# Kernel tuning notes

Hardware: AMD Instinct MI355X
Metric: run time of the kernel (lower is better)

## Reference

```python
import jax, jax.numpy as jnp
import numpy as np

N_NODES = 100000
N_GRAPHS = 1000
NPG = 100           # nodes per graph (fixed)
N_EDGES = 3200000   # avg degree 32
F_IN = 128
K = 30              # SortAggregation k
N_CLASSES = 10


def setup_inputs() -> dict:
    key = jax.random.key(0)
    ks = jax.random.split(key, 24)
    x = jax.random.normal(ks[0], (N_NODES, F_IN), jnp.float32)
    # edges constrained within each 100-node graph
    g = jax.random.randint(ks[1], (N_EDGES,), 0, N_GRAPHS)
    src = g * NPG + jax.random.randint(ks[2], (N_EDGES,), 0, NPG)
    dst = g * NPG + jax.random.randint(ks[3], (N_EDGES,), 0, NPG)
    edge_index = jnp.stack([src, dst]).astype(jnp.int32)
    batch = jnp.repeat(jnp.arange(N_GRAPHS, dtype=jnp.int32), NPG)

    def lin(k, fi, fo):
        return jax.random.normal(k, (fi, fo), jnp.float32) / np.sqrt(fi)

    return {
        "x": x, "edge_index": edge_index, "batch": batch,
        "W1": lin(ks[4], F_IN, 32), "b1": jnp.zeros((32,), jnp.float32),
        "W2": lin(ks[5], 32, 32),   "b2": jnp.zeros((32,), jnp.float32),
        "W3": lin(ks[6], 32, 32),   "b3": jnp.zeros((32,), jnp.float32),
        "W4": lin(ks[7], 32, 1),    "b4": jnp.zeros((1,), jnp.float32),
        "conv5_w": jax.random.normal(ks[8], (16, 1, 97), jnp.float32) / np.sqrt(97.0),
        "conv5_b": jnp.zeros((16,), jnp.float32),
        "conv6_w": jax.random.normal(ks[9], (32, 16, 5), jnp.float32) / np.sqrt(16 * 5.0),
        "conv6_b": jnp.zeros((32,), jnp.float32),
        "fc1_w": lin(ks[10], 352, 128), "fc1_b": jnp.zeros((128,), jnp.float32),
        "fc2_w": lin(ks[11], 128, N_CLASSES), "fc2_b": jnp.zeros((N_CLASSES,), jnp.float32),
    }


def reference(x, edge_index, batch,
              W1, b1, W2, b2, W3, b3, W4, b4,
              conv5_w, conv5_b, conv6_w, conv6_b,
              fc1_w, fc1_b, fc2_w, fc2_b):
    N = x.shape[0]
    src, dst = edge_index[0], edge_index[1]
    # remove_self_loops -> zero edge weight; GCNConv then re-adds self loops (weight 1)
    w = jnp.where(src == dst, 0.0, 1.0).astype(x.dtype)
    deg = jax.ops.segment_sum(w, dst, num_segments=N) + 1.0  # includes self loop
    dis = jax.lax.rsqrt(deg)
    norm = w * dis[src] * dis[dst]        # per-edge D^-1/2 A D^-1/2
    self_norm = dis * dis                 # self-loop coefficient 1/deg

    def gcn(h, W, b):
        h = h @ W                                   # [N, out]
        agg = jax.ops.segment_sum(norm[:, None] * h[src], dst, num_segments=N)
        return agg + self_norm[:, None] * h + b

    x1 = jnp.tanh(gcn(x, W1, b1))
    x2 = jnp.tanh(gcn(x1, W2, b2))
    x3 = jnp.tanh(gcn(x2, W3, b3))
    x4 = jnp.tanh(gcn(x3, W4, b4))
    h = jnp.concatenate([x1, x2, x3, x4], axis=-1)  # [N, 97]
    C = h.shape[-1]

    # SortAggregation(k=30): per graph, sort nodes by last channel descending, keep top k
    xs = h.reshape(N_GRAPHS, NPG, C)
    order = jnp.argsort(-xs[..., -1], axis=1)[:, :K]            # [B, K]
    pooled = jnp.take_along_axis(xs, order[:, :, None], axis=1)  # [B, K, C]
    y = pooled.reshape(N_GRAPHS, 1, K * C)                       # [B, 1, 2910]

    dn = ('NCH', 'OIH', 'NCH')
    y = jax.lax.conv_general_dilated(y, conv5_w, (97,), 'VALID', dimension_numbers=dn)
    y = jax.nn.relu(y + conv5_b[None, :, None])                  # [B, 16, 30]
    B, Co, L = y.shape
    y = y.reshape(B, Co, L // 2, 2).max(axis=-1)                 # maxpool(2,2) -> [B,16,15]
    y = jax.lax.conv_general_dilated(y, conv6_w, (1,), 'VALID', dimension_numbers=dn)
    y = jax.nn.relu(y + conv6_b[None, :, None])                  # [B, 32, 11]
    y = y.reshape(B, -1)                                         # [B, 352]
    out = jax.nn.relu(y @ fc1_w + fc1_b)                         # dropout = identity (eval)
    return jax.nn.log_softmax(out @ fc2_w + fc2_b, axis=-1)
```

## Files before the change

### kernel.cpp

```cpp
#include <hip/hip_runtime.h>

#define N_GRAPHS_C 1000
#define NPG_C      100
#define N_EDGES_C  3200000
#define KTOP_C     30
#define CAP        4096

typedef _Float16 f16x8 __attribute__((ext_vector_type(8)));
typedef float    f32x4 __attribute__((ext_vector_type(4)));

__device__ __forceinline__ unsigned packh2(float x, float y) {
    _Float16 hx = (_Float16)x, hy = (_Float16)y;
    return (unsigned)__builtin_bit_cast(unsigned short, hx) |
           ((unsigned)__builtin_bit_cast(unsigned short, hy) << 16);
}

__device__ __forceinline__ float f16b(unsigned v) {
    return (float)__builtin_bit_cast(_Float16, (unsigned short)v);
}

__device__ __forceinline__ float ftanh(float x) {
    float e = __expf(2.0f * x);
    return 1.0f - 2.0f * __builtin_amdgcn_rcpf(e + 1.0f);
}

__device__ __forceinline__ void split8(const float* v, f16x8& h, f16x8& l) {
    #pragma unroll
    for (int j = 0; j < 8; ++j) {
        _Float16 hh = (_Float16)v[j];
        h[j] = hh;
        l[j] = (_Float16)(v[j] - (float)hh);
    }
}


__global__ __launch_bounds__(1024)
void bucket_kernel(const int* __restrict__ src, const int* __restrict__ dst,
                   int* __restrict__ gcur, unsigned short* __restrict__ slots) {
    __shared__ int hist[N_GRAPHS_C];
    const int tid = threadIdx.x;
    const int base = blockIdx.x * 8192;
    for (int i = tid; i < N_GRAPHS_C; i += 1024) hist[i] = 0;
    __syncthreads();

    int g[8]; unsigned short pk[8]; bool v[8];
    #pragma unroll
    for (int k = 0; k < 8; ++k) {
        int e = base + tid + k * 1024;
        v[k] = false;
        if (e < N_EDGES_C) {
            int s = src[e], d = dst[e];
            if (s != d) {
                int gg = s / NPG_C;
                g[k] = gg;
                pk[k] = (unsigned short)(((d - gg * NPG_C) << 7) | (s - gg * NPG_C));
                v[k] = true;
                atomicAdd(&hist[gg], 1);
            }
        }
    }
    __syncthreads();
    for (int i = tid; i < N_GRAPHS_C; i += 1024) {
        int c = hist[i];
        hist[i] = atomicAdd(&gcur[i], c);
    }
    __syncthreads();
    #pragma unroll
    for (int k = 0; k < 8; ++k) {
        if (v[k]) {
            int pos = atomicAdd(&hist[g[k]], 1);
            if (pos < CAP) slots[g[k] * CAP + pos] = pk[k];
        }
    }
}

__global__ __launch_bounds__(512)
void wprep_kernel(const float* __restrict__ W1, const float* __restrict__ W2,
                  const float* __restrict__ W3, unsigned* __restrict__ wp) {
    const int t = threadIdx.x;
    for (int w = t; w < 2048; w += 512) {
        int n = w >> 6, kp = w & 63, k = kp * 2;
        float a = W1[k*32 + n], b = W1[(k+1)*32 + n];
        _Float16 ah = (_Float16)a, bh = (_Float16)b;
        wp[w]        = (unsigned)__builtin_bit_cast(unsigned short, ah) |
                       ((unsigned)__builtin_bit_cast(unsigned short, bh) << 16);
        wp[2048 + w] = packh2(a - (float)ah, b - (float)bh);
    }
    for (int w = t; w < 512; w += 512) {
        int n = w >> 4, kp = w & 15, k = kp * 2;
        float a = W2[k*32 + n], b = W2[(k+1)*32 + n];
        _Float16 ah = (_Float16)a, bh = (_Float16)b;
        wp[4096 + w] = (unsigned)__builtin_bit_cast(unsigned short, ah) |
                       ((unsigned)__builtin_bit_cast(unsigned short, bh) << 16);
        wp[4608 + w] = packh2(a - (float)ah, b - (float)bh);
    }
    for (int w = t; w < 512; w += 512) {
        int n = w >> 4, kp = w & 15, k = kp * 2;
        float a = W3[k*32 + n], b = W3[(k+1)*32 + n];
        _Float16 ah = (_Float16)a, bh = (_Float16)b;
        wp[5120 + w] = (unsigned)__builtin_bit_cast(unsigned short, ah) |
                       ((unsigned)__builtin_bit_cast(unsigned short, bh) << 16);
        wp[5632 + w] = packh2(a - (float)ah, b - (float)bh);
    }
}

#define SMEM_WORDS 16112

extern "C" __global__ __launch_bounds__(512, 4)
void dgcnn_kernel(const float* __restrict__ x,
                  const int* __restrict__ gcur, const unsigned short* __restrict__ slots,
                  const unsigned* __restrict__ wp,
                  const float* __restrict__ b1, const float* __restrict__ b2,
                  const float* __restrict__ b3,
                  const float* __restrict__ W4, const float* __restrict__ b4,
                  const float* __restrict__ w5, const float* __restrict__ b5,
                  const float* __restrict__ w6, const float* __restrict__ b6,
                  const float* __restrict__ fw1, const float* __restrict__ fb1,
                  const float* __restrict__ fw2, const float* __restrict__ fb2,
                  float* __restrict__ out)
{
    extern __shared__ unsigned smu[];
    unsigned* cntP   = smu;
    unsigned* planes = smu + 7616;
    float* xrows  = (float*)(smu + 11968);
    float* pooled = (float*)(smu + 11968);
    float* dis = (float*)(smu + 15568);
    float* t4  = (float*)(smu + 15680);
    unsigned* t4h = smu + 15784;
    unsigned* t4l = smu + 15848;
    float* sX4 = (float*)(smu + 15912);
    int*   srank = (int*)(smu + 16012);
    float* s5  = (float*)smu;
    float* sPb = s5 + 480;
    float* s6  = s5 + 720;
    float* sO1 = s5 + 1072;
    float* sFc = s5 + 1200;
    float* sZ  = s5 + 1712;
    float* w5s = (float*)(smu + 1728);
    float* b5s = (float*)(smu + 3280);
    float* w6s = (float*)(smu + 3296);
    float* b6s = (float*)(smu + 5856);
    float* fw2s = (float*)(smu + 7616);
    float* fb2s = (float*)(smu + 8896);

    const int tid = threadIdx.x;
    const int g   = blockIdx.x;
    const int l64 = tid & 63;
    const int wv  = tid >> 6;

    const float* xg = x + (size_t)g * NPG_C * 128;
    const unsigned* w1h = wp;
    const unsigned* w1l = wp + 2048;

    for (int idx = tid; idx < 11968; idx += 512) smu[idx] = 0u;
    if (tid < 12) dis[100 + tid] = 0.f;
    if (tid < 100) srank[tid] = 0;
    __syncthreads();

    {
        int ec = gcur[g]; if (ec > CAP) ec = CAP;
        for (int k = tid; k < ec; k += 512) {
            unsigned e = slots[g * CAP + k];
            unsigned idx = (e >> 7) * 104 + (e & 127);
            atomicAdd(&planes[idx >> 2], 1u << ((idx & 3) * 8));
        }
    }
    __syncthreads();

    if (tid < 400) {
        int row = tid >> 2, part = tid & 3;
        int wb = part * 7, we = (part == 3) ? 26 : wb + 7;
        const unsigned* rw = planes + row * 26;
        unsigned s = 0;
        for (int k = wb; k < we; ++k) {
            unsigned v = rw[k];
            s += (v & 0xffu) + ((v >> 8) & 0xffu) + ((v >> 16) & 0xffu) + (v >> 24);
        }
        atomicAdd(&srank[row], (int)s);
    }
    __syncthreads();

    #pragma unroll
    for (int k = 0; k < 6; ++k) {
        int w = tid + k * 512;
        if (w < 2600) {
            unsigned v = planes[w];
            int i = w / 26, c = w - i * 26;
            int d = i * 68 + c * 2;
            cntP[d]     = packh2((float)(v & 255u), (float)((v >> 8) & 255u));
            cntP[d + 1] = packh2((float)((v >> 16) & 255u), (float)(v >> 24));
        }
    }
    if (tid < 100) dis[tid] = rsqrtf((float)srank[tid] + 1.0f);
    __syncthreads();

    auto packStore = [&](f32x4 c, int n, int r0, float4 dv) {
        float v0 = c[0]*dv.x, v1 = c[1]*dv.y, v2 = c[2]*dv.z, v3 = c[3]*dv.w;
        _Float16 h0=(_Float16)v0, h1=(_Float16)v1, h2=(_Float16)v2, h3=(_Float16)v3;
        uint2 wh, wl;
        wh.x = (unsigned)__builtin_bit_cast(unsigned short,h0) |
               ((unsigned)__builtin_bit_cast(unsigned short,h1) << 16);
        wh.y = (unsigned)__builtin_bit_cast(unsigned short,h2) |
               ((unsigned)__builtin_bit_cast(unsigned short,h3) << 16);
        wl.x = packh2(v0-(float)h0, v1-(float)h1);
        wl.y = packh2(v2-(float)h2, v3-(float)h3);
        *(uint2*)&planes[n*68 + (r0>>1)] = wh;
        *(uint2*)&planes[2176 + n*68 + (r0>>1)] = wl;
    };

    for (int idx = tid; idx < 768; idx += 512) {
        int rw = idx / 12, wd = idx - rw * 12;
        planes[rw * 68 + 56 + wd] = 0u;
    }
    if (wv < 7) {
        f32x4 c0 = {0.f,0.f,0.f,0.f}, c1 = {0.f,0.f,0.f,0.f};
        const int arow = (wv << 4) + (l64 & 15);
        const int kq   = (l64 >> 4) << 3;
        const int bn   = l64 & 15;
        const bool aok = arow < 100;
        #pragma unroll
        for (int kc = 0; kc < 4; ++kc) {
            const int kb = (kc << 5) + kq;
            f16x8 ah, al;
            if (aok) {
                float av[8];
                float4 xa = *(const float4*)&xg[arow*128 + kb];
                float4 xb = *(const float4*)&xg[arow*128 + kb + 4];
                av[0]=xa.x; av[1]=xa.y; av[2]=xa.z; av[3]=xa.w;
                av[4]=xb.x; av[5]=xb.y; av[6]=xb.z; av[7]=xb.w;
                split8(av, ah, al);
            } else {
                #pragma unroll
                for (int j = 0; j < 8; ++j) { ah[j] = (_Float16)0.f; al[j] = (_Float16)0.f; }
            }
            f16x8 b0h = __builtin_bit_cast(f16x8, *(const uint4*)(w1h + bn*64 + (kb>>1)));
            f16x8 b0l = __builtin_bit_cast(f16x8, *(const uint4*)(w1l + bn*64 + (kb>>1)));
            f16x8 b1h = __builtin_bit_cast(f16x8, *(const uint4*)(w1h + (bn+16)*64 + (kb>>1)));
            f16x8 b1l = __builtin_bit_cast(f16x8, *(const uint4*)(w1l + (bn+16)*64 + (kb>>1)));
            c0 = __builtin_amdgcn_mfma_f32_16x16x32_f16(ah, b0h, c0, 0, 0, 0);
            c0 = __builtin_amdgcn_mfma_f32_16x16x32_f16(al, b0h, c0, 0, 0, 0);
            c0 = __builtin_amdgcn_mfma_f32_16x16x32_f16(ah, b0l, c0, 0, 0, 0);
            c1 = __builtin_amdgcn_mfma_f32_16x16x32_f16(ah, b1h, c1, 0, 0, 0);
            c1 = __builtin_amdgcn_mfma_f32_16x16x32_f16(al, b1h, c1, 0, 0, 0);
            c1 = __builtin_amdgcn_mfma_f32_16x16x32_f16(ah, b1l, c1, 0, 0, 0);
        }
        const int r0 = (wv << 4) + ((l64 >> 4) << 2);
        float4 dv = *(const float4*)&dis[r0];
        packStore(c0, bn,      r0, dv);
        packStore(c1, bn + 16, r0, dv);
    }
    __syncthreads();

    auto AGG = [&](f32x4& fa, f32x4& fb, const float* Bp, bool wx) {
        if (wv < 7) {
            f32x4 a0 = {0.f,0.f,0.f,0.f}, a1 = {0.f,0.f,0.f,0.f};
            const unsigned* ab = cntP + ((wv << 4) + (l64 & 15)) * 68 + ((l64 >> 4) << 2);
            const unsigned* bb = planes + (l64 & 15) * 68 + ((l64 >> 4) << 2);
            #pragma unroll
            for (int p = 0; p < 2; ++p) {
                const unsigned* bp = bb + p * 2176;
                #pragma unroll
                for (int ks = 0; ks < 4; ++ks) {
                    f16x8 av = __builtin_bit_cast(f16x8, *(const uint4*)(ab + ks*16));
                    f16x8 b0 = __builtin_bit_cast(f16x8, *(const uint4*)(bp + ks*16));
                    f16x8 b1 = __builtin_bit_cast(f16x8, *(const uint4*)(bp + 16*68 + ks*16));
                    a0 = __builtin_amdgcn_mfma_f32_16x16x32_f16(av, b0, a0, 0, 0, 0);
                    a1 = __builtin_amdgcn_mfma_f32_16x16x32_f16(av, b1, a1, 0, 0, 0);
                }
            }
            int n0 = l64 & 15, r0 = (wv << 4) + ((l64 >> 4) << 2);
            uint2 sh0 = *(const uint2*)(planes + n0 * 68 + (r0 >> 1));
            uint2 sl0 = *(const uint2*)(planes + 2176 + n0 * 68 + (r0 >> 1));
            uint2 sh1 = *(const uint2*)(planes + (16 + n0) * 68 + (r0 >> 1));
            uint2 sl1 = *(const uint2*)(planes + 2176 + (16 + n0) * 68 + (r0 >> 1));
            float4 dv = *(const float4*)&dis[r0];
            float bi0 = Bp[n0], bi1 = Bp[16 + n0];
            #pragma unroll
            for (int j = 0; j < 4; ++j) {
                unsigned sft = (unsigned)((j & 1) * 16);
                float sc0 = f16b(((j < 2) ? sh0.x : sh0.y) >> sft) +
                            f16b(((j < 2) ? sl0.x : sl0.y) >> sft);
                float sc1 = f16b(((j < 2) ? sh1.x : sh1.y) >> sft) +
                            f16b(((j < 2) ? sl1.x : sl1.y) >> sft);
                float d_ = (j == 0) ? dv.x : (j == 1) ? dv.y : (j == 2) ? dv.z : dv.w;
                float v0 = ftanh(d_ * (a0[j] + sc0) + bi0);
                float v1 = ftanh(d_ * (a1[j] + sc1) + bi1);
                fa[j] = v0; fb[j] = v1;
                if (wx) {
                    int row = r0 + j;
                    if (row < 100) { xrows[row*36 + n0] = v0; xrows[row*36 + 16 + n0] = v1; }
                }
            }
        }
    };

    auto XWm = [&](const unsigned* wh, const unsigned* wl) {
        if (wv < 7) {
            f32x4 c0 = {0.f,0.f,0.f,0.f}, c1 = {0.f,0.f,0.f,0.f};
            const int arow = (wv << 4) + (l64 & 15);
            const int kq   = (l64 >> 4) << 3;
            const int bn   = l64 & 15;
            f16x8 ah, al;
            if (arow < 100) {
                float av[8];
                float4 xa = *(const float4*)&xrows[arow*36 + kq];
                float4 xb = *(const float4*)&xrows[arow*36 + kq + 4];
                av[0]=xa.x; av[1]=xa.y; av[2]=xa.z; av[3]=xa.w;
                av[4]=xb.x; av[5]=xb.y; av[6]=xb.z; av[7]=xb.w;
                split8(av, ah, al);
            } else {
                #pragma unroll
                for (int j = 0; j < 8; ++j) { ah[j] = (_Float16)0.f; al[j] = (_Float16)0.f; }
            }
            f16x8 b0h = __builtin_bit_cast(f16x8, *(const uint4*)(wh + bn*16 + (kq>>1)));
            f16x8 b0l = __builtin_bit_cast(f16x8, *(const uint4*)(wl + bn*16 + (kq>>1)));
            f16x8 b1h = __builtin_bit_cast(f16x8, *(const uint4*)(wh + (bn+16)*16 + (kq>>1)));
            f16x8 b1l = __builtin_bit_cast(f16x8, *(const uint4*)(wl + (bn+16)*16 + (kq>>1)));
            c0 = __builtin_amdgcn_mfma_f32_16x16x32_f16(ah, b0h, c0, 0, 0, 0);
            c0 = __builtin_amdgcn_mfma_f32_16x16x32_f16(al, b0h, c0, 0, 0, 0);
            c0 = __builtin_amdgcn_mfma_f32_16x16x32_f16(ah, b0l, c0, 0, 0, 0);
            c1 = __builtin_amdgcn_mfma_f32_16x16x32_f16(ah, b1h, c1, 0, 0, 0);
            c1 = __builtin_amdgcn_mfma_f32_16x16x32_f16(al, b1h, c1, 0, 0, 0);
            c1 = __builtin_amdgcn_mfma_f32_16x16x32_f16(ah, b1l, c1, 0, 0, 0);
            const int r0 = (wv << 4) + ((l64 >> 4) << 2);
            float4 dv = *(const float4*)&dis[r0];
            packStore(c0, bn,      r0, dv);
            packStore(c1, bn + 16, r0, dv);
        }
    };

    f32x4 f1a, f1b, f2a, f2b, f3a, f3b;

    AGG(f1a, f1b, b1, true);        __syncthreads();
    XWm(wp + 4096, wp + 4608);      __syncthreads();
    AGG(f2a, f2b, b2, true);        __syncthreads();
    XWm(wp + 5120, wp + 5632);      __syncthreads();
    AGG(f3a, f3b, b3, false);

    if (wv < 7) {
        float w4a = W4[l64 & 15], w4b = W4[16 + (l64 & 15)];
        int r0 = (wv << 4) + ((l64 >> 4) << 2);
        #pragma unroll
        for (int j = 0; j < 4; ++j) {
            float v = f3a[j] * w4a + f3b[j] * w4b;
            v += __shfl_xor(v, 1, 16); v += __shfl_xor(v, 2, 16);
            v += __shfl_xor(v, 4, 16); v += __shfl_xor(v, 8, 16);
            int row = r0 + j;
            if ((l64 & 15) == 0 && row < 100) t4[row] = v * dis[row];
        }
    }
    __syncthreads();

    if (tid < 64) {
        float a = (2*tid < 100) ? t4[2*tid] : 0.f;
        float b = (2*tid+1 < 100) ? t4[2*tid+1] : 0.f;
        _Float16 ah = (_Float16)a, bh = (_Float16)b;
        t4h[tid] = (unsigned)__builtin_bit_cast(unsigned short, ah) |
                   ((unsigned)__builtin_bit_cast(unsigned short, bh) << 16);
        t4l[tid] = packh2(a - (float)ah, b - (float)bh);
    }
    if (tid < 100) srank[tid] = 0;
    __syncthreads();

    if (wv < 7) {
        f32x4 c = {0.f,0.f,0.f,0.f};
        const unsigned* ab = cntP + ((wv << 4) + (l64 & 15)) * 68 + ((l64 >> 4) << 2);
        const int kq = (l64 >> 4) << 3;
        const bool bz = (l64 & 15) == 0;
        #pragma unroll
        for (int ks = 0; ks < 4; ++ks) {
            f16x8 av = __builtin_bit_cast(f16x8, *(const uint4*)(ab + ks*16));
            f16x8 bh, bl;
            if (bz) {
                bh = __builtin_bit_cast(f16x8, *(const uint4*)(t4h + ks*16 + (kq>>1)));
                bl = __builtin_bit_cast(f16x8, *(const uint4*)(t4l + ks*16 + (kq>>1)));
            } else {
                #pragma unroll
                for (int j = 0; j < 8; ++j) { bh[j] = (_Float16)0.f; bl[j] = (_Float16)0.f; }
            }
            c = __builtin_amdgcn_mfma_f32_16x16x32_f16(av, bh, c, 0, 0, 0);
            c = __builtin_amdgcn_mfma_f32_16x16x32_f16(av, bl, c, 0, 0, 0);
        }
        if (bz) {
            int r0 = (wv << 4) + ((l64 >> 4) << 2);
            #pragma unroll
            for (int j = 0; j < 4; ++j) {
                int row = r0 + j;
                if (row < 100) sX4[row] = tanhf(dis[row] * (c[j] + t4[row]) + b4[0]);
            }
        }
    }
    __syncthreads();

    if (tid < 500) {
        int i = tid / 5, seg = tid - i * 5;
        float vi = sX4[i];
        int c = 0, jb = seg * 20;
        #pragma unroll
        for (int jo = 0; jo < 20; ++jo) {
            int j = jb + jo;
            float vj = sX4[j];
            c += (vj > vi) || (vj == vi && j < i);
        }
        atomicAdd(&srank[i], c);
    }
    for (int k = tid; k < 1552; k += 512) w5s[k] = w5[k];
    if (tid < 16)  b5s[tid] = b5[tid];
    for (int k = tid; k < 2560; k += 512) w6s[k] = w6[k];
    if (tid < 32)  b6s[tid] = b6[tid];
    for (int k = tid; k < 1280; k += 512) fw2s[k] = fw2[k];
    if (tid < 10)  fb2s[tid] = fb2[tid];
    __syncthreads();

    if (wv < 7) {
        int n0 = l64 & 15, r0 = (wv << 4) + ((l64 >> 4) << 2);
        #pragma unroll
        for (int j = 0; j < 4; ++j) {
            int row = r0 + j;
            if (row < 100) {
                int rk = srank[row];
                if (rk < KTOP_C) {
                    float* pr = pooled + rk * 100;
                    pr[n0]      = f1a[j]; pr[16 + n0] = f1b[j];
                    pr[32 + n0] = f2a[j]; pr[48 + n0] = f2b[j];
                    pr[64 + n0] = f3a[j]; pr[80 + n0] = f3b[j];
                    if (n0 == 0) pr[96] = sX4[row];
                }
            }
        }
    }
    __syncthreads();

    if (tid < 480) {
        int l = tid >> 4, co = tid & 15;
        const float* pr = pooled + l * 100;
        const float* wr = w5s + co * 97;
        float acc = b5s[co];
        for (int c4 = 0; c4 < 96; c4 += 4) {
            const float4 pv = *(const float4*)&pr[c4];
            acc = fmaf(pv.x, wr[c4+0], fmaf(pv.y, wr[c4+1], fmaf(pv.z, wr[c4+2], fmaf(pv.w, wr[c4+3], acc))));
        }
        acc = fmaf(pr[96], wr[96], acc);
        s5[co * 30 + l] = fmaxf(acc, 0.f);
    }
    __syncthreads();

    if (tid < 240) {
        int co = tid / 15, j = tid - co * 15;
        sPb[co * 15 + j] = fmaxf(s5[co * 30 + 2*j], s5[co * 30 + 2*j + 1]);
    }
    __syncthreads();

    if (tid < 352) {
        int co = tid / 11, l = tid - co * 11;
        float acc = b6s[co];
        for (int ci = 0; ci < 16; ++ci) {
            const float* wr = w6s + (co * 16 + ci) * 5;
            const float* pr = sPb + ci * 15 + l;
            acc = fmaf(wr[0], pr[0], fmaf(wr[1], pr[1], fmaf(wr[2], pr[2],
                  fmaf(wr[3], pr[3], fmaf(wr[4], pr[4], acc)))));
        }
        s6[co * 11 + l] = fmaxf(acc, 0.f);
    }
    __syncthreads();

    {
        int j = tid & 127, part = tid >> 7;
        int ibeg = part * 88, iend = ibeg + 88;
        float acc = (part == 0) ? fb1[j] : 0.f;
        for (int i = ibeg; i < iend; ++i)
            acc = fmaf(s6[i], fw1[i * 128 + j], acc);
        sFc[part * 128 + j] = acc;
    }
    __syncthreads();
    if (tid < 128) {
        float v = sFc[tid] + sFc[128 + tid] + sFc[256 + tid] + sFc[384 + tid];
        sO1[tid] = fmaxf(v, 0.f);
    }
    __syncthreads();

    if (tid < 10) {
        float acc = fb2s[tid];
        for (int k = 0; k < 128; ++k)
            acc = fmaf(sO1[k], fw2s[k * 10 + tid], acc);
        sZ[tid] = acc;
    }
    __syncthreads();
    if (tid < 10) {
        float m = sZ[0];
        for (int c = 1; c < 10; ++c) m = fmaxf(m, sZ[c]);
        float se = 0.f;
        for (int c = 0; c < 10; ++c) se += expf(sZ[c] - m);
        out[g * 10 + tid] = sZ[tid] - m - logf(se);
    }
}

extern "C" void kernel_launch(void* const* d_in, const int* in_sizes, int n_in,
                              void* d_out, int out_size, void* d_ws, size_t ws_size,
                              hipStream_t stream) {
    const float* x   = (const float*)d_in[0];
    const int*   ei  = (const int*)d_in[1];
    const int*   src = ei;
    const int*   dst = ei + N_EDGES_C;
    const float* W1 = (const float*)d_in[3];  const float* b1 = (const float*)d_in[4];
    const float* W2 = (const float*)d_in[5];  const float* b2 = (const float*)d_in[6];
    const float* W3 = (const float*)d_in[7];  const float* b3 = (const float*)d_in[8];
    const float* W4 = (const float*)d_in[9];  const float* b4 = (const float*)d_in[10];
    const float* w5 = (const float*)d_in[11]; const float* b5 = (const float*)d_in[12];
    const float* w6 = (const float*)d_in[13]; const float* b6 = (const float*)d_in[14];
    const float* fw1 = (const float*)d_in[15]; const float* fb1 = (const float*)d_in[16];
    const float* fw2 = (const float*)d_in[17]; const float* fb2 = (const float*)d_in[18];
    float* out = (float*)d_out;

    int* gcur = (int*)d_ws;
    unsigned short* slots = (unsigned short*)((char*)d_ws + 4096);
    unsigned* wpp = (unsigned*)((char*)d_ws + 4096 + (size_t)N_GRAPHS_C * CAP * 2);

    hipMemsetAsync(gcur, 0, 4096, stream);

    bucket_kernel<<<(N_EDGES_C + 8191) / 8192, 1024, 0, stream>>>(src, dst, gcur, slots);
    wprep_kernel<<<1, 512, 0, stream>>>(W1, W2, W3, wpp);

    size_t smem = (size_t)SMEM_WORDS * sizeof(unsigned);
    hipFuncSetAttribute((const void*)dgcnn_kernel,
                        hipFuncAttributeMaxDynamicSharedMemorySize, (int)smem);
    dgcnn_kernel<<<N_GRAPHS_C, 512, smem, stream>>>(
        x, gcur, slots, wpp, b1, b2, b3, W4, b4,
        w5, b5, w6, b6, fw1, fb1, fw2, fb2, out);
}
```

Baseline: 110.1 us.

## Keep adjacency A-fragments in registers and shrink LDS to double occupancy

Removes the fp16 count-matrix copy (cntP) in LDS and instead builds the MFMA A-operand fragments for the adjacency once into registers, reused by all aggregation steps. Conv/FC weights are read directly from global memory instead of being staged into shared memory, cutting the LDS footprint roughly in half and raising launch bounds to 8 blocks per CU. The weight-prep kernel is merged into the bucket kernel as an extra block to save a launch. Risks are higher register pressure from the held fragments and uncached global weight reads in the tail layers.

Result: faster. 106.0 us (-3.7%).

```diff
diff --git a/kernel.cpp b/kernel.cpp
--- a/kernel.cpp
+++ b/kernel.cpp
@@ -5,6 +5,7 @@
 #define N_EDGES_C  3200000
 #define KTOP_C     30
 #define CAP        4096
+#define NB_BUCKET  391
 
 typedef _Float16 f16x8 __attribute__((ext_vector_type(8)));
 typedef float    f32x4 __attribute__((ext_vector_type(4)));
@@ -36,9 +37,36 @@
 
 __global__ __launch_bounds__(1024)
 void bucket_kernel(const int* __restrict__ src, const int* __restrict__ dst,
-                   int* __restrict__ gcur, unsigned short* __restrict__ slots) {
+                   int* __restrict__ gcur, unsigned short* __restrict__ slots,
+                   const float* __restrict__ W1, const float* __restrict__ W2,
+                   const float* __restrict__ W3, unsigned* __restrict__ wp) {
+    const int tid = threadIdx.x;
+    if (blockIdx.x == NB_BUCKET) {
+        for (int w = tid; w < 2048; w += 1024) {
+            int n = w >> 6, kp = w & 63, k = kp * 2;
+            float a = W1[k*32 + n], b = W1[(k+1)*32 + n];
+            _Float16 ah = (_Float16)a, bh = (_Float16)b;
+            wp[w]        = (unsigned)__builtin_bit_cast(unsigned short, ah) |
+                           ((unsigned)__builtin_bit_cast(unsigned short, bh) << 16);
+            wp[2048 + w] = packh2(a - (float)ah, b - (float)bh);
+        }
+        for (int w = tid; w < 512; w += 1024) {
+            int n = w >> 4, kp = w & 15, k = kp * 2;
+            float a = W2[k*32 + n], b = W2[(k+1)*32 + n];
+            _Float16 ah = (_Float16)a, bh = (_Float16)b;
+            wp[4096 + w] = (unsigned)__builtin_bit_cast(unsigned short, ah) |
+                           ((unsigned)__builtin_bit_cast(unsigned short, bh) << 16);
+            wp[4608 + w] = packh2(a - (float)ah, b - (float)bh);
+            float a3 = W3[k*32 + n], b3v = W3[(k+1)*32 + n];
+            _Float16 a3h = (_Float16)a3, b3h = (_Float16)b3v;
+            wp[5120 + w] = (unsigned)__builtin_bit_cast(unsigned short, a3h) |
+                           ((unsigned)__builtin_bit_cast(unsigned short, b3h) << 16);
+            wp[5632 + w] = packh2(a3 - (float)a3h, b3v - (float)b3h);
+        }
+        return;
+    }
+
     __shared__ int hist[N_GRAPHS_C];
-    const int tid = threadIdx.x;
     const int base = blockIdx.x * 8192;
     for (int i = tid; i < N_GRAPHS_C; i += 1024) hist[i] = 0;
     __syncthreads();
@@ -74,39 +102,9 @@
     }
 }
 
-__global__ __launch_bounds__(512)
-void wprep_kernel(const float* __restrict__ W1, const float* __restrict__ W2,
-                  const float* __restrict__ W3, unsigned* __restrict__ wp) {
-    const int t = threadIdx.x;
-    for (int w = t; w < 2048; w += 512) {
-        int n = w >> 6, kp = w & 63, k = kp * 2;
-        float a = W1[k*32 + n], b = W1[(k+1)*32 + n];
-        _Float16 ah = (_Float16)a, bh = (_Float16)b;
-        wp[w]        = (unsigned)__builtin_bit_cast(unsigned short, ah) |
-                       ((unsigned)__builtin_bit_cast(unsigned short, bh) << 16);
-        wp[2048 + w] = packh2(a - (float)ah, b - (float)bh);
-    }
-    for (int w = t; w < 512; w += 512) {
-        int n = w >> 4, kp = w & 15, k = kp * 2;
-        float a = W2[k*32 + n], b = W2[(k+1)*32 + n];
-        _Float16 ah = (_Float16)a, bh = (_Float16)b;
-        wp[4096 + w] = (unsigned)__builtin_bit_cast(unsigned short, ah) |
-                       ((unsigned)__builtin_bit_cast(unsigned short, bh) << 16);
-        wp[4608 + w] = packh2(a - (float)ah, b - (float)bh);
-    }
-    for (int w = t; w < 512; w += 512) {
-        int n = w >> 4, kp = w & 15, k = kp * 2;
-        float a = W3[k*32 + n], b = W3[(k+1)*32 + n];
-        _Float16 ah = (_Float16)a, bh = (_Float16)b;
-        wp[5120 + w] = (unsigned)__builtin_bit_cast(unsigned short, ah) |
-                       ((unsigned)__builtin_bit_cast(unsigned short, bh) << 16);
-        wp[5632 + w] = packh2(a - (float)ah, b - (float)bh);
-    }
-}
-
-#define SMEM_WORDS 16112
-
-extern "C" __global__ __launch_bounds__(512, 4)
+#define SMEM_WORDS 8496
+
+extern "C" __global__ __launch_bounds__(512, 8)
 void dgcnn_kernel(const float* __restrict__ x,
                   const int* __restrict__ gcur, const unsigned short* __restrict__ slots,
                   const unsigned* __restrict__ wp,
@@ -120,28 +118,21 @@
                   float* __restrict__ out)
 {
     extern __shared__ unsigned smu[];
-    unsigned* cntP   = smu;
-    unsigned* planes = smu + 7616;
-    float* xrows  = (float*)(smu + 11968);
-    float* pooled = (float*)(smu + 11968);
-    float* dis = (float*)(smu + 15568);
-    float* t4  = (float*)(smu + 15680);
-    unsigned* t4h = smu + 15784;
-    unsigned* t4l = smu + 15848;
-    float* sX4 = (float*)(smu + 15912);
-    int*   srank = (int*)(smu + 16012);
+    unsigned* planes = smu;
+    float* xrows  = (float*)(smu + 4352);
+    float* pooled = (float*)(smu + 4352);
+    float* dis = (float*)(smu + 7952);
+    float* t4  = (float*)(smu + 8064);
+    unsigned* t4h = smu + 8168;
+    unsigned* t4l = smu + 8232;
+    float* sX4 = (float*)(smu + 8296);
+    int*   srank = (int*)(smu + 8396);
     float* s5  = (float*)smu;
     float* sPb = s5 + 480;
     float* s6  = s5 + 720;
     float* sO1 = s5 + 1072;
     float* sFc = s5 + 1200;
     float* sZ  = s5 + 1712;
-    float* w5s = (float*)(smu + 1728);
-    float* b5s = (float*)(smu + 3280);
-    float* w6s = (float*)(smu + 3296);
-    float* b6s = (float*)(smu + 5856);
-    float* fw2s = (float*)(smu + 7616);
-    float* fb2s = (float*)(smu + 8896);
 
     const int tid = threadIdx.x;
     const int g   = blockIdx.x;
@@ -152,7 +143,7 @@
     const unsigned* w1h = wp;
     const unsigned* w1l = wp + 2048;
 
-    for (int idx = tid; idx < 11968; idx += 512) smu[idx] = 0u;
+    for (int idx = tid; idx < 2600; idx += 512) planes[idx] = 0u;
     if (tid < 12) dis[100 + tid] = 0.f;
     if (tid < 100) srank[tid] = 0;
     __syncthreads();
@@ -178,19 +169,29 @@
         }
         atomicAdd(&srank[row], (int)s);
     }
-    __syncthreads();
-
-    #pragma unroll
-    for (int k = 0; k < 6; ++k) {
-        int w = tid + k * 512;
-        if (w < 2600) {
-            unsigned v = planes[w];
-            int i = w / 26, c = w - i * 26;
-            int d = i * 68 + c * 2;
-            cntP[d]     = packh2((float)(v & 255u), (float)((v >> 8) & 255u));
-            cntP[d + 1] = packh2((float)((v >> 16) & 255u), (float)(v >> 24));
-        }
-    }
+    f16x8 afr[4];
+    {
+        const int arow = (wv << 4) + (l64 & 15);
+        if (wv < 7 && arow < 100) {
+            const unsigned* cb = planes + arow * 26 + ((l64 >> 4) << 1);
+            #pragma unroll
+            for (int ks = 0; ks < 4; ++ks) {
+                uint2 cw = *(const uint2*)(cb + ks * 8);
+                #pragma unroll
+                for (int j = 0; j < 4; ++j) {
+                    afr[ks][j]     = (_Float16)(float)((cw.x >> (8*j)) & 255u);
+                    afr[ks][4 + j] = (_Float16)(float)((cw.y >> (8*j)) & 255u);
+                }
+            }
+        } else {
+            #pragma unroll
+            for (int ks = 0; ks < 4; ++ks)
+                #pragma unroll
+                for (int j = 0; j < 8; ++j) afr[ks][j] = (_Float16)0.f;
+        }
+    }
+    __syncthreads();
+
     if (tid < 100) dis[tid] = rsqrtf((float)srank[tid] + 1.0f);
     __syncthreads();
 
@@ -254,18 +255,16 @@
     auto AGG = [&](f32x4& fa, f32x4& fb, const float* Bp, bool wx) {
         if (wv < 7) {
             f32x4 a0 = {0.f,0.f,0.f,0.f}, a1 = {0.f,0.f,0.f,0.f};
-            const unsigned* ab = cntP + ((wv << 4) + (l64 & 15)) * 68 + ((l64 >> 4) << 2);
             const unsigned* bb = planes + (l64 & 15) * 68 + ((l64 >> 4) << 2);
             #pragma unroll
             for (int p = 0; p < 2; ++p) {
                 const unsigned* bp = bb + p * 2176;
                 #pragma unroll
                 for (int ks = 0; ks < 4; ++ks) {
-                    f16x8 av = __builtin_bit_cast(f16x8, *(const uint4*)(ab + ks*16));
                     f16x8 b0 = __builtin_bit_cast(f16x8, *(const uint4*)(bp + ks*16));
                     f16x8 b1 = __builtin_bit_cast(f16x8, *(const uint4*)(bp + 16*68 + ks*16));
-                    a0 = __builtin_amdgcn_mfma_f32_16x16x32_f16(av, b0, a0, 0, 0, 0);
-                    a1 = __builtin_amdgcn_mfma_f32_16x16x32_f16(av, b1, a1, 0, 0, 0);
+                    a0 = __builtin_amdgcn_mfma_f32_16x16x32_f16(afr[ks], b0, a0, 0, 0, 0);
+                    a1 = __builtin_amdgcn_mfma_f32_16x16x32_f16(afr[ks], b1, a1, 0, 0, 0);
                 }
             }
             int n0 = l64 & 15, r0 = (wv << 4) + ((l64 >> 4) << 2);
@@ -364,22 +363,20 @@
 
     if (wv < 7) {
         f32x4 c = {0.f,0.f,0.f,0.f};
-        const unsigned* ab = cntP + ((wv << 4) + (l64 & 15)) * 68 + ((l64 >> 4) << 2);
-        const int kq = (l64 >> 4) << 3;
+        const int kq2 = (l64 >> 4) << 2;
         const bool bz = (l64 & 15) == 0;
         #pragma unroll
         for (int ks = 0; ks < 4; ++ks) {
-            f16x8 av = __builtin_bit_cast(f16x8, *(const uint4*)(ab + ks*16));
             f16x8 bh, bl;
             if (bz) {
-                bh = __builtin_bit_cast(f16x8, *(const uint4*)(t4h + ks*16 + (kq>>1)));
-                bl = __builtin_bit_cast(f16x8, *(const uint4*)(t4l + ks*16 + (kq>>1)));
+                bh = __builtin_bit_cast(f16x8, *(const uint4*)(t4h + ks*16 + kq2));
+                bl = __builtin_bit_cast(f16x8, *(const uint4*)(t4l + ks*16 + kq2));
             } else {
                 #pragma unroll
                 for (int j = 0; j < 8; ++j) { bh[j] = (_Float16)0.f; bl[j] = (_Float16)0.f; }
             }
-            c = __builtin_amdgcn_mfma_f32_16x16x32_f16(av, bh, c, 0, 0, 0);
-            c = __builtin_amdgcn_mfma_f32_16x16x32_f16(av, bl, c, 0, 0, 0);
+            c = __builtin_amdgcn_mfma_f32_16x16x32_f16(afr[ks], bh, c, 0, 0, 0);
+            c = __builtin_amdgcn_mfma_f32_16x16x32_f16(afr[ks], bl, c, 0, 0, 0);
         }
         if (bz) {
             int r0 = (wv << 4) + ((l64 >> 4) << 2);
@@ -404,12 +401,6 @@
         }
         atomicAdd(&srank[i], c);
     }
-    for (int k = tid; k < 1552; k += 512) w5s[k] = w5[k];
-    if (tid < 16)  b5s[tid] = b5[tid];
-    for (int k = tid; k < 2560; k += 512) w6s[k] = w6[k];
-    if (tid < 32)  b6s[tid] = b6[tid];
-    for (int k = tid; k < 1280; k += 512) fw2s[k] = fw2[k];
-    if (tid < 10)  fb2s[tid] = fb2[tid];
     __syncthreads();
 
     if (wv < 7) {
@@ -434,8 +425,8 @@
     if (tid < 480) {
         int l = tid >> 4, co = tid & 15;
         const float* pr = pooled + l * 100;
-        const float* wr = w5s + co * 97;
-        float acc = b5s[co];
+        const float* wr = w5 + co * 97;
+        float acc = b5[co];
         for (int c4 = 0; c4 < 96; c4 += 4) {
             const float4 pv = *(const float4*)&pr[c4];
             acc = fmaf(pv.x, wr[c4+0], fmaf(pv.y, wr[c4+1], fmaf(pv.z, wr[c4+2], fmaf(pv.w, wr[c4+3], acc))));
@@ -453,9 +444,9 @@
 
     if (tid < 352) {
         int co = tid / 11, l = tid - co * 11;
-        float acc = b6s[co];
+        float acc = b6[co];
         for (int ci = 0; ci < 16; ++ci) {
-            const float* wr = w6s + (co * 16 + ci) * 5;
+            const float* wr = w6 + (co * 16 + ci) * 5;
             const float* pr = sPb + ci * 15 + l;
             acc = fmaf(wr[0], pr[0], fmaf(wr[1], pr[1], fmaf(wr[2], pr[2],
                   fmaf(wr[3], pr[3], fmaf(wr[4], pr[4], acc)))));
@@ -480,9 +471,9 @@
     __syncthreads();
 
     if (tid < 10) {
-        float acc = fb2s[tid];
+        float acc = fb2[tid];
         for (int k = 0; k < 128; ++k)
-            acc = fmaf(sO1[k], fw2s[k * 10 + tid], acc);
+            acc = fmaf(sO1[k], fw2[k * 10 + tid], acc);
         sZ[tid] = acc;
     }
     __syncthreads();
@@ -518,8 +509,8 @@
 
     hipMemsetAsync(gcur, 0, 4096, stream);
 
-    bucket_kernel<<<(N_EDGES_C + 8191) / 8192, 1024, 0, stream>>>(src, dst, gcur, slots);
-    wprep_kernel<<<1, 512, 0, stream>>>(W1, W2, W3, wpp);
+    bucket_kernel<<<NB_BUCKET + 1, 1024, 0, stream>>>(src, dst, gcur, slots,
+                                                      W1, W2, W3, wpp);
 
     size_t smem = (size_t)SMEM_WORDS * sizeof(unsigned);
     hipFuncSetAttribute((const void*)dgcnn_kernel,
```
